# Kernel tuning notes

Hardware: AMD Instinct MI355X
Metric: run time of the kernel (lower is better)

## Reference

```python
import jax, jax.numpy as jnp
import numpy as np

ALPHA = 0.5
BETA = 0.5
THRESHOLD = 0.5


def connected_components(fg):
    """4-connected component labeling (scipy.ndimage.label default structure)
    via iterative min-label propagation. fg: bool [B,H,W]. Returns int32 labels,
    0 = background; foreground labels are arbitrary unique ids per component."""
    B, H, W = fg.shape
    BIG = jnp.int32(H * W + 2)
    idx = (jnp.arange(H * W, dtype=jnp.int32) + 1).reshape(1, H, W)
    labels0 = jnp.where(fg, jnp.broadcast_to(idx, (B, H, W)), 0)

    def nbr_min(l):
        lf = jnp.where(fg, l, BIG)
        up = jnp.concatenate([jnp.full((B, 1, W), BIG, jnp.int32), lf[:, :-1]], 1)
        dn = jnp.concatenate([lf[:, 1:], jnp.full((B, 1, W), BIG, jnp.int32)], 1)
        lt = jnp.concatenate([jnp.full((B, H, 1), BIG, jnp.int32), lf[:, :, :-1]], 2)
        rt = jnp.concatenate([lf[:, :, 1:], jnp.full((B, H, 1), BIG, jnp.int32)], 2)
        m = jnp.minimum(jnp.minimum(up, dn), jnp.minimum(lt, rt))
        return jnp.where(fg, jnp.minimum(lf, m), 0)

    def cond(carry):
        return carry[1]

    def body(carry):
        l, _ = carry
        nl = nbr_min(l)
        return nl, jnp.any(nl != l)

    labels, _ = jax.lax.while_loop(cond, body, (labels0, jnp.bool_(True)))
    return labels


def detect_critical(labels_a, fg_b):
    """Mark every connected component of `labels_a` that contains at least one
    voxel not covered by foreground of the other segmentation (`fg_b`), i.e.
    components touched by a mismatch -> topologically critical. Per-sample."""
    H, W = labels_a.shape
    mismatch = ((labels_a > 0) & (~fg_b)).astype(jnp.int32)
    cnt = jax.ops.segment_sum(mismatch.ravel(), labels_a.ravel(), num_segments=H * W + 1)
    return ((cnt[labels_a] > 0) & (labels_a > 0)).astype(jnp.float32)


def get_critical_masks(pred_bin, target_bin):
    # pred_bin/target_bin: bool [B,H,W]
    pred_lbl = connected_components(pred_bin)
    tgt_lbl = connected_components(target_bin)
    neg = jax.vmap(detect_critical)(tgt_lbl, pred_bin)   # critical comps of target (false-neg)
    pos = jax.vmap(detect_critical)(pred_lbl, target_bin)  # critical comps of pred (false-pos)
    return BETA * neg + (1.0 - BETA) * pos  # [B,H,W]


def setup_inputs() -> dict:
    key = jax.random.key(0)
    k1, k2 = jax.random.split(key)
    B, C, H, W = 8, 1, 512, 512
    preds = jax.random.normal(k1, (B, C, H, W), dtype=jnp.float32)
    targets = (jax.random.uniform(k2, (B, C, H, W)) > 0.5).astype(jnp.float32)
    return {"preds": preds, "targets": targets}


def reference(preds, targets):
    # BCEWithLogitsLoss(reduction='none', pos_weight=1)
    loss = -(targets * jax.nn.log_sigmoid(preds)
             + (1.0 - targets) * jax.nn.log_sigmoid(-preds))  # [B,1,H,W]
    pred_bin = preds[:, 0] > THRESHOLD          # binarize(preds[:,0,...])
    target_bin = targets[:, 0] != 0.0           # scipy.label treats nonzero as fg
    masks = get_critical_masks(pred_bin, target_bin)  # [B,H,W]
    blended = (1.0 - ALPHA) * loss + ALPHA * masks[:, None] * loss
    return blended.mean()
```

## Files before the change

### kernel.cpp

```cpp
#include <hip/hip_runtime.h>
#include <math.h>

#define BATCH 8
#define HH 512
#define WW 512
#define IMG (HH * WW)
#define NTOT (BATCH * IMG)
#define TROWS 4
#define TS (TROWS * WW)
#define NTILES (NTOT / TS)
#define BPF (BATCH * (HH / TROWS - 1) * WW)
#define THRESH 0.5f
#define NBLK (NTOT / 256)


__device__ __forceinline__ int findroot_g(const int* p, int x) {
    int px;
    while ((px = p[x]) != x) x = px;
    return x;
}

__device__ __forceinline__ void unite_g(int* p, int a, int b) {
    bool done = false;
    do {
        a = findroot_g(p, a);
        b = findroot_g(p, b);
        if (a > b) {
            int old = atomicMin(&p[a], b);
            done = (old == a);
            a = old;
        } else if (b > a) {
            int old = atomicMin(&p[b], a);
            done = (old == b);
            b = old;
        } else {
            done = true;
        }
    } while (!done);
}

__device__ __forceinline__ int findroot_s(const int* p, int x) {
    int px;
    while ((px = p[x]) != x) x = px;
    return x;
}

__device__ __forceinline__ void unite_s(int* p, int a, int b) {
    bool done = false;
    do {
        a = findroot_s(p, a);
        b = findroot_s(p, b);
        if (a > b) {
            int old = atomicMin(&p[a], b);
            done = (old == a);
            a = old;
        } else if (b > a) {
            int old = atomicMin(&p[b], a);
            done = (old == b);
            b = old;
        } else {
            done = true;
        }
    } while (!done);
}


__global__ void __launch_bounds__(256) k_local(const float* __restrict__ preds,
                                               const float* __restrict__ targets,
                                               int* __restrict__ pP, int* __restrict__ pT,
                                               unsigned long long* __restrict__ flags64) {
    __shared__ int lp[TS];
    int bid = blockIdx.x;
    int field = bid >> 10;
    int tb = bid & (NTILES - 1);
    const float* __restrict__ src = field ? targets : preds;
    int* __restrict__ gp = field ? pT : pP;
    const int base = tb * TS;

    flags64[bid * 256 + threadIdx.x] = 0ull;

    const float4* __restrict__ src4 = (const float4*)(src + base);
    for (int i = threadIdx.x; i < TS / 4; i += 256) {
        float4 v = src4[i];
        int l = 4 * i;
        if (field) {
            lp[l]     = (v.x != 0.0f) ? l     : -1;
            lp[l + 1] = (v.y != 0.0f) ? l + 1 : -1;
            lp[l + 2] = (v.z != 0.0f) ? l + 2 : -1;
            lp[l + 3] = (v.w != 0.0f) ? l + 3 : -1;
        } else {
            lp[l]     = (v.x > THRESH) ? l     : -1;
            lp[l + 1] = (v.y > THRESH) ? l + 1 : -1;
            lp[l + 2] = (v.z > THRESH) ? l + 2 : -1;
            lp[l + 3] = (v.w > THRESH) ? l + 3 : -1;
        }
    }
    __syncthreads();

    for (int l = threadIdx.x; l < TS; l += 256) {
        if (lp[l] < 0) continue;
        if ((l & (WW - 1)) != WW - 1 && lp[l + 1] >= 0) unite_s(lp, l, l + 1);
        if (l < TS - WW && lp[l + WW] >= 0) unite_s(lp, l, l + WW);
    }
    __syncthreads();

    for (int l = threadIdx.x; l < TS; l += 256) {
        int out = -1;
        if (lp[l] >= 0) out = base + findroot_s(lp, l);
        gp[base + l] = out;
    }
}


__global__ void k_border(int* __restrict__ pP, int* __restrict__ pT) {
    int id = blockIdx.x * blockDim.x + threadIdx.x;
    if (id >= 2 * BPF) return;
    int field = (id >= BPF) ? 1 : 0;
    int r = id - field * BPF;
    int* p = field ? pT : pP;
    const int perimg = (HH / TROWS - 1) * WW;
    int img = r / perimg;
    int rem = r - img * perimg;
    int b = rem >> 9;
    int c = rem & (WW - 1);
    int row = b * TROWS + (TROWS - 1);
    int n = img * IMG + row * WW + c;
    if (p[n] >= 0 && p[n + WW] >= 0) unite_g(p, n, n + WW);
}


__global__ void k_flatmark(int* __restrict__ pP, int* __restrict__ pT,
                           unsigned char* __restrict__ flagP8,
                           unsigned char* __restrict__ flagT8) {
    int n = blockIdx.x * blockDim.x + threadIdx.x;
    if (n >= NTOT) return;
    int a = pP[n];
    int b = pT[n];
    bool fp = a >= 0;
    bool ft = b >= 0;
    if (fp) {
        int r = a, pr;
        while ((pr = pP[r]) != r) r = pr;
        if (a != r) pP[n] = r;
        if (!ft) flagP8[r] = 1;
    }
    if (ft) {
        int r = b, pr;
        while ((pr = pT[r]) != r) r = pr;
        if (b != r) pT[n] = r;
        if (!fp) flagT8[r] = 1;
    }
}


__device__ __forceinline__ float softplusf(float z) {
    return fmaxf(z, 0.0f) + log1pf(expf(-fabsf(z)));
}

__device__ __forceinline__ float block_reduce_sum(float v, float* smem4) {
    for (int off = 32; off > 0; off >>= 1) v += __shfl_down(v, off, 64);
    int lane = threadIdx.x & 63, wid = threadIdx.x >> 6;
    if (lane == 0) smem4[wid] = v;
    __syncthreads();
    return smem4[0] + smem4[1] + smem4[2] + smem4[3];
}

__global__ void k_gather(const float* __restrict__ preds, const float* __restrict__ targets,
                         const int* __restrict__ pP, const int* __restrict__ pT,
                         const unsigned char* __restrict__ flagP8,
                         const unsigned char* __restrict__ flagT8,
                         float* __restrict__ partial) {
    int n = blockIdx.x * blockDim.x + threadIdx.x;
    float contrib = 0.0f;
    if (n < NTOT) {
        float x = preds[n];
        float t = targets[n];
        float loss = t * softplusf(-x) + (1.0f - t) * softplusf(x);
        int a = pP[n];
        int b = pT[n];
        float m = 0.0f;
        if (b >= 0 && flagT8[b]) m += 0.5f;
        if (a >= 0 && flagP8[a]) m += 0.5f;
        contrib = (0.5f + 0.5f * m) * loss;
    }
    __shared__ float smem4[4];
    float s = block_reduce_sum(contrib, smem4);
    if (threadIdx.x == 0) partial[blockIdx.x] = s;
}

__global__ void k_final(const float* __restrict__ partial, float* __restrict__ out) {
    float s = 0.0f;
    for (int i = threadIdx.x; i < NBLK; i += 256) s += partial[i];
    __shared__ float smem4[4];
    float tot = block_reduce_sum(s, smem4);
    if (threadIdx.x == 0) out[0] = tot / (float)NTOT;
}


extern "C" void kernel_launch(void* const* d_in, const int* in_sizes, int n_in,
                              void* d_out, int out_size, void* d_ws, size_t ws_size,
                              hipStream_t stream) {
    const float* preds = (const float*)d_in[0];
    const float* targets = (const float*)d_in[1];

    int* pP = (int*)d_ws;
    int* pT = pP + NTOT;
    unsigned char* flagP8 = (unsigned char*)(pT + NTOT);
    unsigned char* flagT8 = flagP8 + NTOT;
    float* partial = (float*)(flagT8 + NTOT);
    float* out = (float*)d_out;

    const int block = 256;

    k_local<<<2 * NTILES, block, 0, stream>>>(preds, targets, pP, pT,
                                              (unsigned long long*)flagP8);
    k_border<<<(2 * BPF + block - 1) / block, block, 0, stream>>>(pP, pT);
    k_flatmark<<<(NTOT + block - 1) / block, block, 0, stream>>>(pP, pT, flagP8, flagT8);
    k_gather<<<(NTOT + block - 1) / block, block, 0, stream>>>(preds, targets, pP, pT, flagP8, flagT8, partial);
    k_final<<<1, 256, 0, stream>>>(partial, out);
}
```

Before: 82.14 us.

## Use wave-ballot run-length labeling and pruned vertical unions in local CCL

Replaces per-pixel horizontal union-find in the tile labeling kernel with a wavefront ballot that links each foreground pixel directly to the start of its horizontal run. Vertical unions are skipped when the left and lower-left neighbours are both foreground, since that connection is already implied. The border kernel unites the stored root labels directly instead of the pixel indices. This aims to cut atomic union traffic and path chasing in shared memory, at the cost of relying on cross-wave reads of neighbour signs.

```diff
diff --git a/kernel.cpp b/kernel.cpp
--- a/kernel.cpp
+++ b/kernel.cpp
@@ -97,10 +97,30 @@
     }
     __syncthreads();
 
+    const int lane = threadIdx.x & 63;
+
     for (int l = threadIdx.x; l < TS; l += 256) {
-        if (lp[l] < 0) continue;
-        if ((l & (WW - 1)) != WW - 1 && lp[l + 1] >= 0) unite_s(lp, l, l + 1);
-        if (l < TS - WW && lp[l + WW] >= 0) unite_s(lp, l, l + WW);
+        int wbase = l & ~63;
+        bool fg = lp[l] >= 0;
+        unsigned long long m = __ballot(fg);
+        int col0 = wbase & (WW - 1);
+        bool left0 = (col0 != 0) && (lp[wbase - 1] >= 0);
+        unsigned long long starts = m & ~(m << 1);
+        if (left0) starts &= ~1ull;
+        unsigned long long below = starts & (~0ull >> (63 - lane));
+        if (fg) {
+            int dst = below ? (wbase + (63 - __clzll(below)))
+                            : (wbase - 1);
+            lp[l] = dst;
+        }
+    }
+    __syncthreads();
+
+    for (int l = threadIdx.x; l < TS - WW; l += 256) {
+        if (lp[l] < 0 || lp[l + WW] < 0) continue;
+        int col = l & (WW - 1);
+        if (col != 0 && lp[l - 1] >= 0 && lp[l + WW - 1] >= 0) continue;
+        unite_s(lp, l, l + WW);
     }
     __syncthreads();
 
@@ -125,7 +145,9 @@
     int c = rem & (WW - 1);
     int row = b * TROWS + (TROWS - 1);
     int n = img * IMG + row * WW + c;
-    if (p[n] >= 0 && p[n + WW] >= 0) unite_g(p, n, n + WW);
+    int ra = p[n];
+    int rb = p[n + WW];
+    if (ra >= 0 && rb >= 0) unite_g(p, ra, rb);
 }
 
 
@@ -215,7 +237,7 @@
     k_local<<<2 * NTILES, block, 0, stream>>>(preds, targets, pP, pT,
                                               (unsigned long long*)flagP8);
     k_border<<<(2 * BPF + block - 1) / block, block, 0, stream>>>(pP, pT);
-    k_flatmark<<<(NTOT + block - 1) / block, block, 0, stream>>>(pP, pT, flagP8, flagT8);
-    k_gather<<<(NTOT + block - 1) / block, block, 0, stream>>>(preds, targets, pP, pT, flagP8, flagT8, partial);
+    k_flatmark<<<NBLK, block, 0, stream>>>(pP, pT, flagP8, flagT8);
+    k_gather<<<NBLK, block, 0, stream>>>(preds, targets, pP, pT, flagP8, flagT8, partial);
     k_final<<<1, 256, 0, stream>>>(partial, out);
 }
```

Result: faster. 76.29 us (-7.1%).
